# Performance work log

Measured on AMD Instinct MI355X. Metric: run time of the kernel, lower is better.

## Reference

```python
import jax, jax.numpy as jnp
import numpy as np


def setup_inputs() -> dict:
    key = jax.random.key(0)
    ks = jax.random.split(key, 7)
    B, S, C, H, W = 4, 8, 256, 64, 64
    A = 256
    return {
        "x": jax.random.normal(ks[0], (B, S, C, H, W), dtype=jnp.float32),
        "wq": jax.random.normal(ks[1], (A, C), dtype=jnp.float32) * (1.0 / np.sqrt(C)),
        "bq": jax.random.normal(ks[2], (A,), dtype=jnp.float32) * 0.01,
        "wk": jax.random.normal(ks[3], (A, C), dtype=jnp.float32) * (1.0 / np.sqrt(C)),
        "bk": jax.random.normal(ks[4], (A,), dtype=jnp.float32) * 0.01,
        "wv": jax.random.normal(ks[5], (A, C), dtype=jnp.float32) * (1.0 / np.sqrt(C)),
        "bv": jax.random.normal(ks[6], (A,), dtype=jnp.float32) * 0.01,
    }


def reference(x, wq, bq, wk, bk, wv, bv):
    B, S, C, H, W = x.shape
    A = wq.shape[0]
    HW = H * W
    scale = 1.0 / (A ** 0.5)

    # 1x1 conv == channel GEMM over flattened spatial dims: [B*S, C, HW] -> [B*S, A, HW]
    xr = x.reshape(B * S, C, HW)
    q = jnp.einsum('ncp,ac->nap', xr, wq) + bq[None, :, None]
    k = jnp.einsum('ncp,ac->nap', xr, wk) + bk[None, :, None]
    v = jnp.einsum('ncp,ac->nap', xr, wv) + bv[None, :, None]

    # [B, S, A, HW]
    q = q.reshape(B, S, A, HW)
    k = k.reshape(B, S, A, HW)
    v = v.reshape(B, S, A, HW)

    # Faithful to torch permute+contiguous().view: raw row-major reinterpretation
    # of the trailing [A, S] block as [S, A] (not a transpose).
    q = jnp.transpose(q, (0, 3, 2, 1)).reshape(B * HW, S, A)
    k = jnp.transpose(k, (0, 3, 1, 2)).reshape(B * HW, A, S)
    v = jnp.transpose(v, (0, 3, 2, 1)).reshape(B * HW, S, A)

    scores = jnp.einsum('nsa,nat->nst', q, k) * scale  # [B*HW, S, S]
    weights = jax.nn.softmax(scores, axis=-1)
    attended = jnp.einsum('nst,nta->nsa', weights, v)  # [B*HW, S, A]

    # view(B, H, W, A, S) raw reshape, then permute(0,4,3,1,2) -> [B, S, A, H, W]
    attended = attended.reshape(B, H, W, A, S)
    attended = jnp.transpose(attended, (0, 4, 3, 1, 2)).reshape(B, S, A, H, W)
    return attended
```

## Files before the change

### kernel.cpp

```cpp
#include <hip/hip_runtime.h>
#include <hip/hip_bf16.h>

typedef __hip_bfloat16 bf16;
typedef __attribute__((ext_vector_type(8))) short short8;
typedef __attribute__((ext_vector_type(4))) float f32x4;

#define MFMA16(A, B, C) __builtin_amdgcn_mfma_f32_16x16x32_bf16((A), (B), (C), 0, 0, 0)

__device__ __forceinline__ unsigned pkbf(float a, float b) {
    __hip_bfloat162 h2 = __float22bfloat162_rn(make_float2(a, b));
    return *reinterpret_cast<unsigned*>(&h2);
}

__global__ __launch_bounds__(256) void prep_w(const float* __restrict__ wq,
                                              const float* __restrict__ wk,
                                              const float* __restrict__ wv,
                                              bf16* __restrict__ wsW)
{
    const int t = (int)blockIdx.x * 256 + (int)threadIdx.x;
    const int lane = t & 63, kk = (t >> 6) & 7, mt = (t >> 9) & 15, proj = t >> 13;
    const float* W = (proj == 0) ? wq : ((proj == 1) ? wk : wv);
    const int row = mt * 16 + (lane & 15);
    const int col = kk * 32 + (lane >> 4) * 8;
    bf16* dst = wsW + (size_t)t * 8;
#pragma unroll
    for (int j = 0; j < 8; ++j) dst[j] = __float2bfloat16(W[row * 256 + col + j]);
}

#define QLB 8192
#define KLB 41984
#define VLB 8192
#define PLB 75776

__global__ __launch_bounds__(512, 4)
void fused_sa(const float* __restrict__ x,
              const float* __restrict__ bq, const float* __restrict__ bk,
              const float* __restrict__ bv,
              const bf16* __restrict__ wsW,
              float* __restrict__ out)
{
    __shared__ __align__(16) char SM[76928];

    const int tid = (int)threadIdx.x;
    const int l = tid & 63, w = tid >> 6, h = l >> 4, c15 = l & 15;
    const int p = c15 & 7, beta = c15 >> 3;

    const int wg = ((int)blockIdx.x & 7) * 256 + ((int)blockIdx.x >> 3);
    const int b = wg >> 9, p0 = (wg & 511) * 8;

    const short8* wsv = (const short8*)wsW;
    const int p2 = (l & 3) * 2, chi = l >> 2;
    const size_t xbase = ((size_t)((b * 8 + w) * 256)) * 4096 + p0 + p2;

    f32x4 aQ0[4] = {}, aQ1[4] = {}, aK0[4] = {}, aK1[4] = {};
    {
        float2 xr[4];
#pragma unroll
        for (int i = 0; i < 4; ++i)
            xr[i] = *(const float2*)&x[xbase + (size_t)(i * 16 + chi) * 4096];

        for (int cc = 0; cc < 4; ++cc) {
            if (cc) __syncthreads();
#pragma unroll
            for (int i = 0; i < 4; ++i) {
                const int c = i * 16 + chi;
                const int r0 = w * 8 + p2, r1 = r0 + 1;
                *(bf16*)(SM + ((r0 * 128 + c * 2) ^ ((r0 & 7) << 4))) = __float2bfloat16(xr[i].x);
                *(bf16*)(SM + ((r1 * 128 + c * 2) ^ ((r1 & 7) << 4))) = __float2bfloat16(xr[i].y);
            }
            if (cc < 3) {
#pragma unroll
                for (int i = 0; i < 4; ++i)
                    xr[i] = *(const float2*)&x[xbase + (size_t)((cc + 1) * 64 + i * 16 + chi) * 4096];
            }
            __syncthreads();
#pragma unroll
            for (int k2 = 0; k2 < 2; ++k2) {
                const int kg = cc * 2 + k2;
                const short8 fQ0 = wsv[((0 * 16 + 2 * w)     * 8 + kg) * 64 + l];
                const short8 fQ1 = wsv[((0 * 16 + 2 * w + 1) * 8 + kg) * 64 + l];
                const short8 fK0 = wsv[((1 * 16 + 2 * w)     * 8 + kg) * 64 + l];
                const short8 fK1 = wsv[((1 * 16 + 2 * w + 1) * 8 + kg) * 64 + l];
#pragma unroll
                for (int nt = 0; nt < 4; ++nt) {
                    const int row = nt * 16 + c15;
                    const short8 bx = *(const short8*)(SM +
                        ((row * 128 + (k2 * 32 + h * 8) * 2) ^ ((row & 7) << 4)));
                    aQ0[nt] = MFMA16(fQ0, bx, aQ0[nt]);
                    aQ1[nt] = MFMA16(fQ1, bx, aQ1[nt]);
                    aK0[nt] = MFMA16(fK0, bx, aK0[nt]);
                    aK1[nt] = MFMA16(fK1, bx, aK1[nt]);
                }
            }
        }
    }

    {
        const float4 b0 = *(const float4*)&bq[(2 * w) * 16 + 4 * h];
        const float4 b1 = *(const float4*)&bq[(2 * w + 1) * 16 + 4 * h];
        const float b0v[4] = {b0.x, b0.y, b0.z, b0.w}, b1v[4] = {b1.x, b1.y, b1.z, b1.w};
#pragma unroll
        for (int r = 0; r < 4; ++r) {
            unsigned wds[4];
#pragma unroll
            for (int nt = 0; nt < 4; ++nt) {
                const float a0 = aQ0[nt][r] + b0v[r];
                const float a1 = aQ1[nt][r] + b1v[r];
                const float send = beta ? a0 : a1;
                const float recv = __shfl_xor(send, 8);
                const float own  = beta ? a1 : a0;
                wds[nt] = beta ? pkbf(recv, own) : pkbf(own, recv);
            }
            const int G = 16 * beta + 4 * h + r;
            *(uint4*)(SM + QLB + ((p * 4224 + w * 528 + G * 16) ^ ((p & 7) << 4))) =
                make_uint4(wds[0], wds[1], wds[2], wds[3]);
        }
    }
    {
        const float4 b0 = *(const float4*)&bk[(2 * w) * 16 + 4 * h];
        const float4 b1 = *(const float4*)&bk[(2 * w + 1) * 16 + 4 * h];
        const float b0v[4] = {b0.x, b0.y, b0.z, b0.w}, b1v[4] = {b1.x, b1.y, b1.z, b1.w};
        const bool lower = (h < 2);
#pragma unroll
        for (int r = 0; r < 4; ++r) {
            const int t = 4 * (h & 1) + r;
#pragma unroll
            for (int nt = 0; nt < 4; ++nt) {
                const float a0 = aK0[nt][r] + b0v[r];
                const float a1 = aK1[nt][r] + b1v[r];
                const float r0 = __shfl_xor(a0, 32);
                const float r1 = __shfl_xor(a1, 32);
                const float j0 = lower ? a0 : r0;
                const float j1 = lower ? r0 : a0;
                const float j2 = lower ? a1 : r1;
                const float j3 = lower ? r1 : a1;
                if ((nt & 1) == (h >> 1)) {
                    const int a = ((2 * nt + beta) * 4 + (w >> 1)) * 8 + (w & 1) * 4;
                    *(uint2*)(SM + KLB + ((p * 4224 + t * 528 + a * 2) ^ ((p & 7) << 4))) =
                        make_uint2(pkbf(j0, j1), pkbf(j2, j3));
                }
            }
        }
    }
    __syncthreads();

    if (w < 4) {
        const int q = w, pxr = c15 >> 3, st = c15 & 7;
        const int px = 2 * q + pxr;
        f32x4 sacc = {0.f, 0.f, 0.f, 0.f};
#pragma unroll
        for (int kk = 0; kk < 8; ++kk) {
            const int off = (px * 4224 + st * 528 + (kk * 32 + h * 8) * 2) ^ ((px & 7) << 4);
            const short8 qa = *(const short8*)(SM + QLB + off);
            const short8 kb = *(const short8*)(SM + KLB + off);
            sacc = MFMA16(qa, kb, sacc);
        }
        const bool valid = ((h >> 1) == pxr);
        const int pxo = 2 * q + (h >> 1);
        bf16 (*PL)[9][8] = (bf16 (*)[9][8])(SM + PLB);
#pragma unroll
        for (int r = 0; r < 4; ++r) {
            const float S = sacc[r] * 0.0625f;
            float m = S;
            m = fmaxf(m, __shfl_xor(m, 1));
            m = fmaxf(m, __shfl_xor(m, 2));
            m = fmaxf(m, __shfl_xor(m, 4));
            const float e = __expf(S - m);
            float sm = e;
            sm += __shfl_xor(sm, 1);
            sm += __shfl_xor(sm, 2);
            sm += __shfl_xor(sm, 4);
            if (valid) PL[pxo][4 * (h & 1) + r][st] = __float2bfloat16(e / sm);
        }
    }
    __syncthreads();

    const int Mv = ((w >> 1) << 2) | (w & 1);
    f32x4 aV0[4] = {}, aV1[4] = {};
    {
        float2 xr[4];
#pragma unroll
        for (int i = 0; i < 4; ++i)
            xr[i] = *(const float2*)&x[xbase + (size_t)(i * 16 + chi) * 4096];

        for (int cc = 0; cc < 4; ++cc) {
            __syncthreads();
#pragma unroll
            for (int i = 0; i < 4; ++i) {
                const int c = i * 16 + chi;
                const int r0 = w * 8 + p2, r1 = r0 + 1;
                *(bf16*)(SM + ((r0 * 128 + c * 2) ^ ((r0 & 7) << 4))) = __float2bfloat16(xr[i].x);
                *(bf16*)(SM + ((r1 * 128 + c * 2) ^ ((r1 & 7) << 4))) = __float2bfloat16(xr[i].y);
            }
            if (cc < 3) {
#pragma unroll
                for (int i = 0; i < 4; ++i)
                    xr[i] = *(const float2*)&x[xbase + (size_t)((cc + 1) * 64 + i * 16 + chi) * 4096];
            }
            __syncthreads();
#pragma unroll
            for (int k2 = 0; k2 < 2; ++k2) {
                const int kg = cc * 2 + k2;
                const short8 fV0 = wsv[((2 * 16 + Mv)     * 8 + kg) * 64 + l];
                const short8 fV1 = wsv[((2 * 16 + Mv + 2) * 8 + kg) * 64 + l];
#pragma unroll
                for (int nt = 0; nt < 4; ++nt) {
                    const int row = nt * 16 + c15;
                    const short8 bx = *(const short8*)(SM +
                        ((row * 128 + (k2 * 32 + h * 8) * 2) ^ ((row & 7) << 4)));
                    aV0[nt] = MFMA16(fV0, bx, aV0[nt]);
                    aV1[nt] = MFMA16(fV1, bx, aV1[nt]);
                }
            }
        }
    }

    {
        const float4 b0 = *(const float4*)&bv[Mv * 16 + 4 * h];
        const float4 b1 = *(const float4*)&bv[(Mv + 2) * 16 + 4 * h];
        const float b0v[4] = {b0.x, b0.y, b0.z, b0.w}, b1v[4] = {b1.x, b1.y, b1.z, b1.w};
        const int tp2 = 2 * (w >> 1);
#pragma unroll
        for (int r = 0; r < 4; ++r)
#pragma unroll
            for (int nt = 0; nt < 4; ++nt) {
                const unsigned wd = pkbf(aV0[nt][r] + b0v[r], aV1[nt][r] + b1v[r]);
                const int aV = (16 * (w & 1) + 4 * h + r) * 8 + 2 * nt + beta;
                *(unsigned*)(SM + VLB +
                    ((p * 4096 + aV * 16 + tp2 * 2) ^ (((p ^ (aV >> 3)) & 7) << 4))) = wd;
            }
    }
    __syncthreads();

    {
        bf16 (*PL)[9][8] = (bf16 (*)[9][8])(SM + PLB);
        const int pxl = c15 & 3, sl = c15 >> 2;
        const short8 zv = {0, 0, 0, 0, 0, 0, 0, 0};
#pragma unroll
        for (int sg = 0; sg < 2; ++sg) {
            short8 pa[2];
#pragma unroll
            for (int q = 0; q < 2; ++q) {
                const short8 t8 = *(const short8*)&PL[q * 4 + pxl][sg * 4 + sl][0];
                pa[q] = (h == pxl) ? t8 : zv;
            }
            const int s = sg * 4 + h;
#pragma unroll
            for (int ci = 0; ci < 2; ++ci) {
                const int a = (2 * w + ci) * 16 + c15;
                const int s2 = a & 7, a2 = (s << 5) | (a >> 3);
#pragma unroll
                for (int q = 0; q < 2; ++q) {
                    const int px = q * 4 + h;
                    const short8 vb = *(const short8*)(SM + VLB +
                        ((px * 4096 + a * 16) ^ (((px ^ (a >> 3)) & 7) << 4)));
                    f32x4 pacc = {0.f, 0.f, 0.f, 0.f};
                    pacc = MFMA16(pa[q], vb, pacc);
                    *(f32x4*)&out[((size_t)((b * 8 + s2) * 256 + a2)) * 4096 + p0 + q * 4] = pacc;
                }
            }
        }
    }
}

extern "C" void kernel_launch(void* const* d_in, const int* in_sizes, int n_in,
                              void* d_out, int out_size, void* d_ws, size_t ws_size,
                              hipStream_t stream) {
    (void)in_sizes; (void)n_in; (void)out_size; (void)ws_size;
    const float* x  = (const float*)d_in[0];
    const float* wq = (const float*)d_in[1];
    const float* bq = (const float*)d_in[2];
    const float* wk = (const float*)d_in[3];
    const float* bk = (const float*)d_in[4];
    const float* wv = (const float*)d_in[5];
    const float* bv = (const float*)d_in[6];
    float* out = (float*)d_out;
    bf16* wsW  = (bf16*)d_ws;

    hipLaunchKernelGGL(prep_w, dim3(96), dim3(256), 0, stream, wq, wk, wv, wsW);
    hipLaunchKernelGGL(fused_sa, dim3(2048), dim3(512), 0, stream,
                       x, bq, bk, bv, wsW, out);
}
```

Before: 183.8 us.

## Stage full x tile in LDS once and reuse for Q/K and V projections

The x tile for all 256 channels is loaded once into LDS as bf16 and kept resident, so the V projection reuses it instead of re-reading x from global memory in four chunks. This removes the duplicate global load of x and many chunk barriers. To make room, the Q/K staging buffers are halved and the scores and softmax phase runs in two passes over pixel halves. That adds barriers and register pressure from holding 16 float2 loads per thread, and it makes less overlap between loads and MFMA work.

```diff
diff --git a/kernel.cpp b/kernel.cpp
--- a/kernel.cpp
+++ b/kernel.cpp
@@ -27,10 +27,10 @@
     for (int j = 0; j < 8; ++j) dst[j] = __float2bfloat16(W[row * 256 + col + j]);
 }
 
-#define QLB 8192
-#define KLB 41984
-#define VLB 8192
-#define PLB 75776
+#define VLB 0
+#define QLB 32768
+#define KLB 49664
+#define PLB 66560
 
 __global__ __launch_bounds__(512, 4)
 void fused_sa(const float* __restrict__ x,
@@ -39,7 +39,7 @@
               const bf16* __restrict__ wsW,
               float* __restrict__ out)
 {
-    __shared__ __align__(16) char SM[76928];
+    __shared__ __align__(16) char SM[67712];
 
     const int tid = (int)threadIdx.x;
     const int l = tid & 63, w = tid >> 6, h = l >> 4, c15 = l & 15;
@@ -49,171 +49,143 @@
     const int b = wg >> 9, p0 = (wg & 511) * 8;
 
     const short8* wsv = (const short8*)wsW;
-    const int p2 = (l & 3) * 2, chi = l >> 2;
-    const size_t xbase = ((size_t)((b * 8 + w) * 256)) * 4096 + p0 + p2;
+
+    {
+        const int p2 = (l & 3) * 2, chi = l >> 2;
+        const size_t xbase = ((size_t)((b * 8 + w) * 256)) * 4096 + p0 + p2;
+        float2 xr[16];
+#pragma unroll
+        for (int i = 0; i < 16; ++i)
+            xr[i] = *(const float2*)&x[xbase + (size_t)(i * 16 + chi) * 4096];
+        const int r0 = w * 8 + p2, r1 = r0 + 1;
+#pragma unroll
+        for (int i = 0; i < 16; ++i) {
+            const int c = i * 16 + chi;
+            *(bf16*)(SM + ((r0 * 512 + c * 2) ^ ((r0 & 7) << 4))) = __float2bfloat16(xr[i].x);
+            *(bf16*)(SM + ((r1 * 512 + c * 2) ^ ((r1 & 7) << 4))) = __float2bfloat16(xr[i].y);
+        }
+    }
+    __syncthreads();
 
     f32x4 aQ0[4] = {}, aQ1[4] = {}, aK0[4] = {}, aK1[4] = {};
-    {
-        float2 xr[4];
-#pragma unroll
-        for (int i = 0; i < 4; ++i)
-            xr[i] = *(const float2*)&x[xbase + (size_t)(i * 16 + chi) * 4096];
-
-        for (int cc = 0; cc < 4; ++cc) {
-            if (cc) __syncthreads();
-#pragma unroll
-            for (int i = 0; i < 4; ++i) {
-                const int c = i * 16 + chi;
-                const int r0 = w * 8 + p2, r1 = r0 + 1;
-                *(bf16*)(SM + ((r0 * 128 + c * 2) ^ ((r0 & 7) << 4))) = __float2bfloat16(xr[i].x);
-                *(bf16*)(SM + ((r1 * 128 + c * 2) ^ ((r1 & 7) << 4))) = __float2bfloat16(xr[i].y);
-            }
-            if (cc < 3) {
-#pragma unroll
-                for (int i = 0; i < 4; ++i)
-                    xr[i] = *(const float2*)&x[xbase + (size_t)((cc + 1) * 64 + i * 16 + chi) * 4096];
-            }
-            __syncthreads();
-#pragma unroll
-            for (int k2 = 0; k2 < 2; ++k2) {
-                const int kg = cc * 2 + k2;
-                const short8 fQ0 = wsv[((0 * 16 + 2 * w)     * 8 + kg) * 64 + l];
-                const short8 fQ1 = wsv[((0 * 16 + 2 * w + 1) * 8 + kg) * 64 + l];
-                const short8 fK0 = wsv[((1 * 16 + 2 * w)     * 8 + kg) * 64 + l];
-                const short8 fK1 = wsv[((1 * 16 + 2 * w + 1) * 8 + kg) * 64 + l];
-#pragma unroll
-                for (int nt = 0; nt < 4; ++nt) {
-                    const int row = nt * 16 + c15;
-                    const short8 bx = *(const short8*)(SM +
-                        ((row * 128 + (k2 * 32 + h * 8) * 2) ^ ((row & 7) << 4)));
-                    aQ0[nt] = MFMA16(fQ0, bx, aQ0[nt]);
-                    aQ1[nt] = MFMA16(fQ1, bx, aQ1[nt]);
-                    aK0[nt] = MFMA16(fK0, bx, aK0[nt]);
-                    aK1[nt] = MFMA16(fK1, bx, aK1[nt]);
-                }
-            }
-        }
-    }
-
-    {
-        const float4 b0 = *(const float4*)&bq[(2 * w) * 16 + 4 * h];
-        const float4 b1 = *(const float4*)&bq[(2 * w + 1) * 16 + 4 * h];
-        const float b0v[4] = {b0.x, b0.y, b0.z, b0.w}, b1v[4] = {b1.x, b1.y, b1.z, b1.w};
+#pragma unroll
+    for (int kg = 0; kg < 8; ++kg) {
+        const short8 fQ0 = wsv[((0 * 16 + 2 * w)     * 8 + kg) * 64 + l];
+        const short8 fQ1 = wsv[((0 * 16 + 2 * w + 1) * 8 + kg) * 64 + l];
+        const short8 fK0 = wsv[((1 * 16 + 2 * w)     * 8 + kg) * 64 + l];
+        const short8 fK1 = wsv[((1 * 16 + 2 * w + 1) * 8 + kg) * 64 + l];
+#pragma unroll
+        for (int nt = 0; nt < 4; ++nt) {
+            const int row = nt * 16 + c15;
+            const short8 bx = *(const short8*)(SM +
+                ((row * 512 + (kg * 32 + h * 8) * 2) ^ ((row & 7) << 4)));
+            aQ0[nt] = MFMA16(fQ0, bx, aQ0[nt]);
+            aQ1[nt] = MFMA16(fQ1, bx, aQ1[nt]);
+            aK0[nt] = MFMA16(fK0, bx, aK0[nt]);
+            aK1[nt] = MFMA16(fK1, bx, aK1[nt]);
+        }
+    }
+
+    const float4 bq0 = *(const float4*)&bq[(2 * w) * 16 + 4 * h];
+    const float4 bq1 = *(const float4*)&bq[(2 * w + 1) * 16 + 4 * h];
+    const float4 bk0 = *(const float4*)&bk[(2 * w) * 16 + 4 * h];
+    const float4 bk1 = *(const float4*)&bk[(2 * w + 1) * 16 + 4 * h];
+    const float bq0v[4] = {bq0.x, bq0.y, bq0.z, bq0.w}, bq1v[4] = {bq1.x, bq1.y, bq1.z, bq1.w};
+    const float bk0v[4] = {bk0.x, bk0.y, bk0.z, bk0.w}, bk1v[4] = {bk1.x, bk1.y, bk1.z, bk1.w};
+
+#pragma unroll
+    for (int half = 0; half < 2; ++half) {
 #pragma unroll
         for (int r = 0; r < 4; ++r) {
             unsigned wds[4];
 #pragma unroll
             for (int nt = 0; nt < 4; ++nt) {
-                const float a0 = aQ0[nt][r] + b0v[r];
-                const float a1 = aQ1[nt][r] + b1v[r];
+                const float a0 = aQ0[nt][r] + bq0v[r];
+                const float a1 = aQ1[nt][r] + bq1v[r];
                 const float send = beta ? a0 : a1;
                 const float recv = __shfl_xor(send, 8);
                 const float own  = beta ? a1 : a0;
                 wds[nt] = beta ? pkbf(recv, own) : pkbf(own, recv);
             }
-            const int G = 16 * beta + 4 * h + r;
-            *(uint4*)(SM + QLB + ((p * 4224 + w * 528 + G * 16) ^ ((p & 7) << 4))) =
-                make_uint4(wds[0], wds[1], wds[2], wds[3]);
-        }
-    }
-    {
-        const float4 b0 = *(const float4*)&bk[(2 * w) * 16 + 4 * h];
-        const float4 b1 = *(const float4*)&bk[(2 * w + 1) * 16 + 4 * h];
-        const float b0v[4] = {b0.x, b0.y, b0.z, b0.w}, b1v[4] = {b1.x, b1.y, b1.z, b1.w};
-        const bool lower = (h < 2);
-#pragma unroll
-        for (int r = 0; r < 4; ++r) {
-            const int t = 4 * (h & 1) + r;
-#pragma unroll
-            for (int nt = 0; nt < 4; ++nt) {
-                const float a0 = aK0[nt][r] + b0v[r];
-                const float a1 = aK1[nt][r] + b1v[r];
-                const float r0 = __shfl_xor(a0, 32);
-                const float r1 = __shfl_xor(a1, 32);
-                const float j0 = lower ? a0 : r0;
-                const float j1 = lower ? r0 : a0;
-                const float j2 = lower ? a1 : r1;
-                const float j3 = lower ? r1 : a1;
-                if ((nt & 1) == (h >> 1)) {
-                    const int a = ((2 * nt + beta) * 4 + (w >> 1)) * 8 + (w & 1) * 4;
-                    *(uint2*)(SM + KLB + ((p * 4224 + t * 528 + a * 2) ^ ((p & 7) << 4))) =
-                        make_uint2(pkbf(j0, j1), pkbf(j2, j3));
+            if ((p >> 2) == half) {
+                const int G = 16 * beta + 4 * h + r;
+                *(uint4*)(SM + QLB + (((p & 3) * 4224 + w * 528 + G * 16) ^ ((p & 7) << 4))) =
+                    make_uint4(wds[0], wds[1], wds[2], wds[3]);
+            }
+        }
+        {
+            const bool lower = (h < 2);
+#pragma unroll
+            for (int r = 0; r < 4; ++r) {
+                const int t = 4 * (h & 1) + r;
+#pragma unroll
+                for (int nt = 0; nt < 4; ++nt) {
+                    const float a0 = aK0[nt][r] + bk0v[r];
+                    const float a1 = aK1[nt][r] + bk1v[r];
+                    const float r0 = __shfl_xor(a0, 32);
+                    const float r1 = __shfl_xor(a1, 32);
+                    const float j0 = lower ? a0 : r0;
+                    const float j1 = lower ? r0 : a0;
+                    const float j2 = lower ? a1 : r1;
+                    const float j3 = lower ? r1 : a1;
+                    if (((nt & 1) == (h >> 1)) && ((p >> 2) == half)) {
+                        const int a = ((2 * nt + beta) * 4 + (w >> 1)) * 8 + (w & 1) * 4;
+                        *(uint2*)(SM + KLB + (((p & 3) * 4224 + t * 528 + a * 2) ^ ((p & 7) << 4))) =
+                            make_uint2(pkbf(j0, j1), pkbf(j2, j3));
+                    }
                 }
             }
         }
-    }
-    __syncthreads();
-
-    if (w < 4) {
-        const int q = w, pxr = c15 >> 3, st = c15 & 7;
-        const int px = 2 * q + pxr;
-        f32x4 sacc = {0.f, 0.f, 0.f, 0.f};
-#pragma unroll
-        for (int kk = 0; kk < 8; ++kk) {
-            const int off = (px * 4224 + st * 528 + (kk * 32 + h * 8) * 2) ^ ((px & 7) << 4);
-            const short8 qa = *(const short8*)(SM + QLB + off);
-            const short8 kb = *(const short8*)(SM + KLB + off);
-            sacc = MFMA16(qa, kb, sacc);
-        }
-        const bool valid = ((h >> 1) == pxr);
-        const int pxo = 2 * q + (h >> 1);
-        bf16 (*PL)[9][8] = (bf16 (*)[9][8])(SM + PLB);
-#pragma unroll
-        for (int r = 0; r < 4; ++r) {
-            const float S = sacc[r] * 0.0625f;
-            float m = S;
-            m = fmaxf(m, __shfl_xor(m, 1));
-            m = fmaxf(m, __shfl_xor(m, 2));
-            m = fmaxf(m, __shfl_xor(m, 4));
-            const float e = __expf(S - m);
-            float sm = e;
-            sm += __shfl_xor(sm, 1);
-            sm += __shfl_xor(sm, 2);
-            sm += __shfl_xor(sm, 4);
-            if (valid) PL[pxo][4 * (h & 1) + r][st] = __float2bfloat16(e / sm);
-        }
-    }
-    __syncthreads();
+        __syncthreads();
+
+        if ((w >> 1) == half) {
+            const int pxr = c15 >> 3, st = c15 & 7;
+            const int px = 2 * w + pxr;
+            f32x4 sacc = {0.f, 0.f, 0.f, 0.f};
+#pragma unroll
+            for (int kk = 0; kk < 8; ++kk) {
+                const int off = ((px & 3) * 4224 + st * 528 + (kk * 32 + h * 8) * 2) ^ ((px & 7) << 4);
+                const short8 qa = *(const short8*)(SM + QLB + off);
+                const short8 kb = *(const short8*)(SM + KLB + off);
+                sacc = MFMA16(qa, kb, sacc);
+            }
+            const bool valid = ((h >> 1) == pxr);
+            const int pxo = 2 * w + (h >> 1);
+            bf16 (*PL)[9][8] = (bf16 (*)[9][8])(SM + PLB);
+#pragma unroll
+            for (int r = 0; r < 4; ++r) {
+                const float S = sacc[r] * 0.0625f;
+                float m = S;
+                m = fmaxf(m, __shfl_xor(m, 1));
+                m = fmaxf(m, __shfl_xor(m, 2));
+                m = fmaxf(m, __shfl_xor(m, 4));
+                const float e = __expf(S - m);
+                float sm = e;
+                sm += __shfl_xor(sm, 1);
+                sm += __shfl_xor(sm, 2);
+                sm += __shfl_xor(sm, 4);
+                if (valid) PL[pxo][4 * (h & 1) + r][st] = __float2bfloat16(e / sm);
+            }
+        }
+        if (half == 0) __syncthreads();
+    }
 
     const int Mv = ((w >> 1) << 2) | (w & 1);
     f32x4 aV0[4] = {}, aV1[4] = {};
-    {
-        float2 xr[4];
-#pragma unroll
-        for (int i = 0; i < 4; ++i)
-            xr[i] = *(const float2*)&x[xbase + (size_t)(i * 16 + chi) * 4096];
-
-        for (int cc = 0; cc < 4; ++cc) {
-            __syncthreads();
-#pragma unroll
-            for (int i = 0; i < 4; ++i) {
-                const int c = i * 16 + chi;
-                const int r0 = w * 8 + p2, r1 = r0 + 1;
-                *(bf16*)(SM + ((r0 * 128 + c * 2) ^ ((r0 & 7) << 4))) = __float2bfloat16(xr[i].x);
-                *(bf16*)(SM + ((r1 * 128 + c * 2) ^ ((r1 & 7) << 4))) = __float2bfloat16(xr[i].y);
-            }
-            if (cc < 3) {
-#pragma unroll
-                for (int i = 0; i < 4; ++i)
-                    xr[i] = *(const float2*)&x[xbase + (size_t)((cc + 1) * 64 + i * 16 + chi) * 4096];
-            }
-            __syncthreads();
-#pragma unroll
-            for (int k2 = 0; k2 < 2; ++k2) {
-                const int kg = cc * 2 + k2;
-                const short8 fV0 = wsv[((2 * 16 + Mv)     * 8 + kg) * 64 + l];
-                const short8 fV1 = wsv[((2 * 16 + Mv + 2) * 8 + kg) * 64 + l];
-#pragma unroll
-                for (int nt = 0; nt < 4; ++nt) {
-                    const int row = nt * 16 + c15;
-                    const short8 bx = *(const short8*)(SM +
-                        ((row * 128 + (k2 * 32 + h * 8) * 2) ^ ((row & 7) << 4)));
-                    aV0[nt] = MFMA16(fV0, bx, aV0[nt]);
-                    aV1[nt] = MFMA16(fV1, bx, aV1[nt]);
-                }
-            }
-        }
-    }
+#pragma unroll
+    for (int kg = 0; kg < 8; ++kg) {
+        const short8 fV0 = wsv[((2 * 16 + Mv)     * 8 + kg) * 64 + l];
+        const short8 fV1 = wsv[((2 * 16 + Mv + 2) * 8 + kg) * 64 + l];
+#pragma unroll
+        for (int nt = 0; nt < 4; ++nt) {
+            const int row = nt * 16 + c15;
+            const short8 bx = *(const short8*)(SM +
+                ((row * 512 + (kg * 32 + h * 8) * 2) ^ ((row & 7) << 4)));
+            aV0[nt] = MFMA16(fV0, bx, aV0[nt]);
+            aV1[nt] = MFMA16(fV1, bx, aV1[nt]);
+        }
+    }
+    __syncthreads();
 
     {
         const float4 b0 = *(const float4*)&bv[Mv * 16 + 4 * h];
```

Result: slower. 241.2 us (+31.2%).
